# Performance work log

Hardware: AMD Instinct MI355X
Metric: run time of the kernel (lower is better)

## Reference

```python
import jax, jax.numpy as jnp
import numpy as np

B, L = 128, 4096
H, RH, D, K = 128, 64, 64, 512  # num_hiddens, residual_hiddens, embedding_dim, num_embeddings
BETA = 0.25  # commitment_cost


def conv1d(x, w, b=None, stride=1, pad=0):
    # x: (N, C, W); w: (O, I, K) torch layout
    y = jax.lax.conv_general_dilated(x, w, (stride,), [(pad, pad)],
                                     dimension_numbers=('NCW', 'OIW', 'NCW'))
    return y if b is None else y + b[None, :, None]


def convT1d(x, w, b=None, stride=2, pad=1):
    # torch ConvTranspose1d weight layout (in, out, k)
    k = w.shape[-1]
    w_t = jnp.flip(w, -1).transpose(1, 0, 2)  # (out, in, k)
    y = jax.lax.conv_general_dilated(x, w_t, (1,), [(k - 1 - pad, k - 1 - pad)],
                                     lhs_dilation=(stride,),
                                     dimension_numbers=('NCW', 'OIW', 'NCW'))
    return y if b is None else y + b[None, :, None]


def res_stack(x, layers):
    for w1, w2 in layers:
        h = conv1d(jax.nn.relu(x), w1, None, 1, 1)
        h = conv1d(jax.nn.relu(h), w2, None, 1, 0)
        x = x + h
    return jax.nn.relu(x)


def _forward(x, enc_w1, enc_b1, enc_w2, enc_b2, enc_w3, enc_b3,
             enc_r1a, enc_r1b, enc_r2a, enc_r2b, pre_vq_w, pre_vq_b, codebook,
             dec_w1, dec_b1, dec_r1a, dec_r1b, dec_r2a, dec_r2b,
             dec_ct1_w, dec_ct1_b, dec_ct2_w, dec_ct2_b):
    # ---- Encoder (compression_factor == 4) ----
    h = x[:, None, :]                                   # (B, 1, L)
    h = jax.nn.relu(conv1d(h, enc_w1, enc_b1, 2, 1))    # (B, H/2, L/2)
    h = jax.nn.relu(conv1d(h, enc_w2, enc_b2, 2, 1))    # (B, H, L/4)
    h = conv1d(h, enc_w3, enc_b3, 1, 1)
    h = res_stack(h, [(enc_r1a, enc_r1b), (enc_r2a, enc_r2b)])
    z = conv1d(h, pre_vq_w, pre_vq_b, 1, 0)             # (B, D, T)

    # ---- Vector quantization ----
    zt = z.transpose(0, 2, 1)                           # (B, T, D)
    flat = zt.reshape(-1, D)                            # (BT, D)
    dists = (jnp.sum(flat * flat, 1, keepdims=True)
             - 2.0 * flat @ codebook.T
             + jnp.sum(codebook * codebook, 1))         # (BT, K)
    idx = jnp.argmin(dists, axis=1)                     # (BT,)
    q = codebook[idx].reshape(zt.shape)                 # (B, T, D)

    e_latent = jnp.mean((jax.lax.stop_gradient(q) - zt) ** 2)
    q_latent = jnp.mean((q - jax.lax.stop_gradient(zt)) ** 2)
    loss = q_latent + BETA * e_latent
    q_st = zt + jax.lax.stop_gradient(q - zt)           # straight-through

    counts = jnp.zeros((K,), flat.dtype).at[idx].add(1.0)
    probs = counts / idx.shape[0]
    perplexity = jnp.exp(-jnp.sum(probs * jnp.log(probs + 1e-10)))

    # ---- Decoder (compression_factor == 4) ----
    hd = q_st.transpose(0, 2, 1)                        # (B, D, T)
    hd = conv1d(hd, dec_w1, dec_b1, 1, 1)               # (B, H, T)
    hd = res_stack(hd, [(dec_r1a, dec_r1b), (dec_r2a, dec_r2b)])
    hd = jax.nn.relu(convT1d(hd, dec_ct1_w, dec_ct1_b)) # (B, H/2, 2T)
    hd = convT1d(hd, dec_ct2_w, dec_ct2_b)              # (B, 1, 4T)
    recon = jnp.squeeze(hd)                             # (B, L)
    return loss, recon, perplexity


def setup_inputs() -> dict:
    key = jax.random.key(0)
    ks = jax.random.split(key, 32)
    n = lambda i, shape, s=0.05: jax.random.normal(ks[i], shape, jnp.float32) * s
    inp = {
        'x': jax.random.normal(ks[0], (B, L), jnp.float32),
        'enc_w1': n(1, (H // 2, 1, 4)), 'enc_b1': jnp.zeros((H // 2,), jnp.float32),
        'enc_w2': n(2, (H, H // 2, 4)), 'enc_b2': jnp.zeros((H,), jnp.float32),
        'enc_w3': n(3, (H, H, 3)), 'enc_b3': jnp.zeros((H,), jnp.float32),
        'enc_r1a': n(4, (RH, H, 3)), 'enc_r1b': n(5, (H, RH, 1)),
        'enc_r2a': n(6, (RH, H, 3)), 'enc_r2b': n(7, (H, RH, 1)),
        'pre_vq_w': n(8, (D, H, 1)), 'pre_vq_b': jnp.zeros((D,), jnp.float32),
        'codebook': jax.random.uniform(ks[9], (K, D), jnp.float32, -1.0 / K, 1.0 / K),
        'dec_w1': n(10, (H, D, 3)), 'dec_b1': jnp.zeros((H,), jnp.float32),
        'dec_r1a': n(11, (RH, H, 3)), 'dec_r1b': n(12, (H, RH, 1)),
        'dec_r2a': n(13, (RH, H, 3)), 'dec_r2b': n(14, (H, RH, 1)),
        'dec_ct1_w': n(15, (H, H // 2, 4)), 'dec_ct1_b': jnp.zeros((H // 2,), jnp.float32),
        'dec_ct2_w': n(16, (H // 2, 1, 4)), 'dec_ct2_b': jnp.zeros((1,), jnp.float32),
    }
    return inp


def reference(x, enc_w1, enc_b1, enc_w2, enc_b2, enc_w3, enc_b3,
              enc_r1a, enc_r1b, enc_r2a, enc_r2b, pre_vq_w, pre_vq_b, codebook,
              dec_w1, dec_b1, dec_r1a, dec_r1b, dec_r2a, dec_r2b,
              dec_ct1_w, dec_ct1_b, dec_ct2_w, dec_ct2_b):
    return _forward(x, enc_w1, enc_b1, enc_w2, enc_b2, enc_w3, enc_b3,
                    enc_r1a, enc_r1b, enc_r2a, enc_r2b, pre_vq_w, pre_vq_b, codebook,
                    dec_w1, dec_b1, dec_r1a, dec_r1b, dec_r2a, dec_r2b,
                    dec_ct1_w, dec_ct1_b, dec_ct2_w, dec_ct2_b)
```

## Files before the change

### kernel.cpp

```cpp
#include <hip/hip_runtime.h>
#include <hip/hip_bf16.h>
#include <math.h>

using bf16 = __hip_bfloat16;
typedef __attribute__((ext_vector_type(4))) float f32x4;
typedef __attribute__((ext_vector_type(8))) short s16x8;

#define MFMA16(a,b,c) __builtin_amdgcn_mfma_f32_16x16x32_bf16((a),(b),(c),0,0,0)


__device__ inline float bf2f(unsigned short u) {
    union { float f; unsigned v; } c; c.v = ((unsigned)u) << 16; return c.f;
}
__device__ inline unsigned short bfbits(float f) {
    union { bf16 h; unsigned short u; } c; c.h = __float2bfloat16(f); return c.u;
}
__device__ inline s16x8 relu8(s16x8 v) {
#pragma unroll
    for (int j = 0; j < 8; ++j)
        v[j] = (short)(((unsigned short)v[j] & 0x8000u) ? 0 : (unsigned short)v[j]);
    return v;
}

__global__ __launch_bounds__(256) void encmid_k(
    const bf16* __restrict__ in, const bf16* __restrict__ w3t,
    const float* __restrict__ b3, const bf16* __restrict__ r1w1,
    const bf16* __restrict__ r1w2, const bf16* __restrict__ r2w1,
    const bf16* __restrict__ r2w2, bf16* __restrict__ out)
{
    __shared__ bf16 sX[96 * 128];
    __shared__ bf16 sY[80 * 128];
    __shared__ bf16 sH[80 * 64];
    const int tid = threadIdx.x;
    const int b   = blockIdx.y;
    const int l0  = blockIdx.x * 64;
    const bf16* inb = in + (size_t)b * 1024 * 128;

    for (int i = tid; i < 96 * 16; i += 256) {
        int t = i >> 4, c0 = (i & 15) * 8;
        int g = l0 - 16 + t;
        s16x8 v = {};
        if (g >= 0 && g < 1024) v = *(const s16x8*)(inb + (size_t)g * 128 + c0);
        int byte = ((t * 128 + c0) << 1) ^ ((t & 7) << 4);
        *(s16x8*)((char*)sX + byte) = v;
    }
    __syncthreads();

    const int lane = tid & 63;
    const int wid  = __builtin_amdgcn_readfirstlane(tid >> 6);
    const int lr   = lane & 15;
    const int kg   = lane >> 4;
    const f32x4 zf4 = {0.f, 0.f, 0.f, 0.f};

    {
        const int co0 = wid * 32;
        f32x4 acc[2][5];
#pragma unroll
        for (int cf = 0; cf < 2; ++cf)
#pragma unroll
            for (int lf = 0; lf < 5; ++lf) acc[cf][lf] = zf4;
#pragma unroll
        for (int k = 0; k < 3; ++k) {
            const bf16* Ab = w3t + (size_t)k * 128 * 128;
#pragma unroll
            for (int ks = 0; ks < 4; ++ks) {
                s16x8 af[2];
#pragma unroll
                for (int cf = 0; cf < 2; ++cf)
                    af[cf] = *(const s16x8*)(Ab + (co0 + cf * 16 + lr) * 128 + ks * 32 + kg * 8);
                s16x8 bfr[5];
#pragma unroll
                for (int lf = 0; lf < 5; ++lf) {
                    int tx = lf * 16 + lr + 7 + k;
                    int byte = ((tx * 128 + ks * 32 + kg * 8) << 1) ^ ((tx & 7) << 4);
                    bfr[lf] = *(const s16x8*)((const char*)sX + byte);
                }
#pragma unroll
                for (int cf = 0; cf < 2; ++cf)
#pragma unroll
                    for (int lf = 0; lf < 5; ++lf)
                        acc[cf][lf] = MFMA16(af[cf], bfr[lf], acc[cf][lf]);
            }
        }
#pragma unroll
        for (int cf = 0; cf < 2; ++cf)
#pragma unroll
            for (int lf = 0; lf < 5; ++lf) {
                int row = lf * 16 + lr;
                int p   = l0 - 8 + row;
                int cb0 = co0 + cf * 16 + kg * 4;
                bool ok = (p >= 0 && p < 1024);
                float r[4];
#pragma unroll
                for (int j = 0; j < 4; ++j)
                    r[j] = ok ? (acc[cf][lf][j] + b3[cb0 + j]) : 0.f;
                uint2 pk;
                pk.x = (unsigned)bfbits(r[0]) | ((unsigned)bfbits(r[1]) << 16);
                pk.y = (unsigned)bfbits(r[2]) | ((unsigned)bfbits(r[3]) << 16);
                int byte = ((row * 128 + cb0) << 1) ^ ((row & 7) << 4);
                *(uint2*)((char*)sY + byte) = pk;
            }
    }
    __syncthreads();

#pragma unroll 1
    for (int blk = 0; blk < 2; ++blk) {
        const bf16* w1 = blk ? r2w1 : r1w1;
        {
            const int co0 = wid * 16;
            f32x4 acc[5];
#pragma unroll
            for (int lf = 0; lf < 5; ++lf) acc[lf] = zf4;
#pragma unroll
            for (int k = 0; k < 3; ++k) {
                const bf16* Ab = w1 + (size_t)k * 64 * 128;
#pragma unroll
                for (int ks = 0; ks < 4; ++ks) {
                    s16x8 a = *(const s16x8*)(Ab + (co0 + lr) * 128 + ks * 32 + kg * 8);
                    s16x8 bfr[5];
#pragma unroll
                    for (int lf = 0; lf < 5; ++lf) {
                        int ry = lf * 16 + lr + k - 1;
                        ry = (ry < 0) ? 0 : (ry > 79 ? 79 : ry);
                        int byte = ((ry * 128 + ks * 32 + kg * 8) << 1) ^ ((ry & 7) << 4);
                        bfr[lf] = relu8(*(const s16x8*)((const char*)sY + byte));
                    }
#pragma unroll
                    for (int lf = 0; lf < 5; ++lf)
                        acc[lf] = MFMA16(a, bfr[lf], acc[lf]);
                }
            }
#pragma unroll
            for (int lf = 0; lf < 5; ++lf) {
                int row = lf * 16 + lr;
                int ch0 = co0 + kg * 4;
                uint2 pk;
                pk.x = (unsigned)bfbits(fmaxf(acc[lf][0], 0.f)) |
                       ((unsigned)bfbits(fmaxf(acc[lf][1], 0.f)) << 16);
                pk.y = (unsigned)bfbits(fmaxf(acc[lf][2], 0.f)) |
                       ((unsigned)bfbits(fmaxf(acc[lf][3], 0.f)) << 16);
                int byte = ((row * 64 + ch0) << 1) ^ ((row & 7) << 4);
                *(uint2*)((char*)sH + byte) = pk;
            }
        }
        __syncthreads();

        if (blk == 0) {
            const int co0 = wid * 32;
            f32x4 acc[2][5];
#pragma unroll
            for (int cf = 0; cf < 2; ++cf)
#pragma unroll
                for (int lf = 0; lf < 5; ++lf) acc[cf][lf] = zf4;
#pragma unroll
            for (int ks = 0; ks < 2; ++ks) {
                s16x8 af[2];
#pragma unroll
                for (int cf = 0; cf < 2; ++cf)
                    af[cf] = *(const s16x8*)(r1w2 + (size_t)(co0 + cf * 16 + lr) * 64 + ks * 32 + kg * 8);
                s16x8 bfr[5];
#pragma unroll
                for (int lf = 0; lf < 5; ++lf) {
                    int row = lf * 16 + lr;
                    int byte = ((row * 64 + ks * 32 + kg * 8) << 1) ^ ((row & 7) << 4);
                    bfr[lf] = *(const s16x8*)((const char*)sH + byte);
                }
#pragma unroll
                for (int cf = 0; cf < 2; ++cf)
#pragma unroll
                    for (int lf = 0; lf < 5; ++lf)
                        acc[cf][lf] = MFMA16(af[cf], bfr[lf], acc[cf][lf]);
            }
#pragma unroll
            for (int cf = 0; cf < 2; ++cf)
#pragma unroll
                for (int lf = 0; lf < 5; ++lf) {
                    int row = lf * 16 + lr;
                    int p   = l0 - 8 + row;
                    int cb0 = co0 + cf * 16 + kg * 4;
                    int byte = ((row * 128 + cb0) << 1) ^ ((row & 7) << 4);
                    uint2 old = *(const uint2*)((const char*)sY + byte);
                    bool ok = (p >= 0 && p < 1024);
                    float r[4];
                    r[0] = acc[cf][lf][0] + bf2f((unsigned short)(old.x & 0xffff));
                    r[1] = acc[cf][lf][1] + bf2f((unsigned short)(old.x >> 16));
                    r[2] = acc[cf][lf][2] + bf2f((unsigned short)(old.y & 0xffff));
                    r[3] = acc[cf][lf][3] + bf2f((unsigned short)(old.y >> 16));
                    uint2 pk;
                    pk.x = ok ? ((unsigned)bfbits(r[0]) | ((unsigned)bfbits(r[1]) << 16)) : 0u;
                    pk.y = ok ? ((unsigned)bfbits(r[2]) | ((unsigned)bfbits(r[3]) << 16)) : 0u;
                    *(uint2*)((char*)sY + byte) = pk;
                }
            __syncthreads();
        } else {
            const int co0 = wid * 32;
            f32x4 acc[2][4];
#pragma unroll
            for (int cf = 0; cf < 2; ++cf)
#pragma unroll
                for (int lf = 0; lf < 4; ++lf) acc[cf][lf] = zf4;
#pragma unroll
            for (int ks = 0; ks < 2; ++ks) {
                s16x8 af[2];
#pragma unroll
                for (int cf = 0; cf < 2; ++cf)
                    af[cf] = *(const s16x8*)(r2w2 + (size_t)(co0 + cf * 16 + lr) * 64 + ks * 32 + kg * 8);
                s16x8 bfr[4];
#pragma unroll
                for (int lf = 0; lf < 4; ++lf) {
                    int row = 8 + lf * 16 + lr;
                    int byte = ((row * 64 + ks * 32 + kg * 8) << 1) ^ ((row & 7) << 4);
                    bfr[lf] = *(const s16x8*)((const char*)sH + byte);
                }
#pragma unroll
                for (int cf = 0; cf < 2; ++cf)
#pragma unroll
                    for (int lf = 0; lf < 4; ++lf)
                        acc[cf][lf] = MFMA16(af[cf], bfr[lf], acc[cf][lf]);
            }
#pragma unroll
            for (int cf = 0; cf < 2; ++cf)
#pragma unroll
                for (int lf = 0; lf < 4; ++lf) {
                    int row = 8 + lf * 16 + lr;
                    int cb0 = co0 + cf * 16 + kg * 4;
                    int byte = ((row * 128 + cb0) << 1) ^ ((row & 7) << 4);
                    uint2 old = *(const uint2*)((const char*)sY + byte);
                    float r[4];
                    r[0] = fmaxf(acc[cf][lf][0] + bf2f((unsigned short)(old.x & 0xffff)), 0.f);
                    r[1] = fmaxf(acc[cf][lf][1] + bf2f((unsigned short)(old.x >> 16)), 0.f);
                    r[2] = fmaxf(acc[cf][lf][2] + bf2f((unsigned short)(old.y & 0xffff)), 0.f);
                    r[3] = fmaxf(acc[cf][lf][3] + bf2f((unsigned short)(old.y >> 16)), 0.f);
                    uint2 pk;
                    pk.x = (unsigned)bfbits(r[0]) | ((unsigned)bfbits(r[1]) << 16);
                    pk.y = (unsigned)bfbits(r[2]) | ((unsigned)bfbits(r[3]) << 16);
                    *(uint2*)(out + ((size_t)b * 1024 + l0 + lf * 16 + lr) * 128 + cb0) = pk;
                }
        }
    }
}

__global__ __launch_bounds__(256) void decmid_k(
    const bf16* __restrict__ qin, const bf16* __restrict__ dw1,
    const float* __restrict__ db1, const bf16* __restrict__ r1w1,
    const bf16* __restrict__ r1w2, const bf16* __restrict__ r2w1,
    const bf16* __restrict__ r2w2, const bf16* __restrict__ ct1w,
    const float* __restrict__ ct1b, bf16* __restrict__ out)
{
    __shared__ bf16 sQ[96 * 64];
    __shared__ bf16 sY[80 * 128];
    __shared__ bf16 sH[80 * 64];
    const int tid = threadIdx.x;
    const int b   = blockIdx.y;
    const int l0  = blockIdx.x * 64;
    const bf16* inb = qin + (size_t)b * 1024 * 64;

    for (int i = tid; i < 96 * 8; i += 256) {
        int t = i >> 3, c0 = (i & 7) * 8;
        int g = l0 - 16 + t;
        s16x8 v = {};
        if (g >= 0 && g < 1024) v = *(const s16x8*)(inb + (size_t)g * 64 + c0);
        int byte = ((t * 64 + c0) << 1) ^ ((t & 7) << 4);
        *(s16x8*)((char*)sQ + byte) = v;
    }
    __syncthreads();

    const int lane = tid & 63;
    const int wid  = __builtin_amdgcn_readfirstlane(tid >> 6);
    const int lr   = lane & 15;
    const int kg   = lane >> 4;
    const f32x4 zf4 = {0.f, 0.f, 0.f, 0.f};

    {
        const int co0 = wid * 32;
        f32x4 acc[2][5];
#pragma unroll
        for (int cf = 0; cf < 2; ++cf)
#pragma unroll
            for (int lf = 0; lf < 5; ++lf) acc[cf][lf] = zf4;
#pragma unroll
        for (int k = 0; k < 3; ++k) {
            const bf16* Ab = dw1 + (size_t)k * 128 * 64;
#pragma unroll
            for (int ks = 0; ks < 2; ++ks) {
                s16x8 af[2];
#pragma unroll
                for (int cf = 0; cf < 2; ++cf)
                    af[cf] = *(const s16x8*)(Ab + (co0 + cf * 16 + lr) * 64 + ks * 32 + kg * 8);
                s16x8 bfr[5];
#pragma unroll
                for (int lf = 0; lf < 5; ++lf) {
                    int tx = lf * 16 + lr + 7 + k;
                    int byte = ((tx * 64 + ks * 32 + kg * 8) << 1) ^ ((tx & 7) << 4);
                    bfr[lf] = *(const s16x8*)((const char*)sQ + byte);
                }
#pragma unroll
                for (int cf = 0; cf < 2; ++cf)
#pragma unroll
                    for (int lf = 0; lf < 5; ++lf)
                        acc[cf][lf] = MFMA16(af[cf], bfr[lf], acc[cf][lf]);
            }
        }
#pragma unroll
        for (int cf = 0; cf < 2; ++cf)
#pragma unroll
            for (int lf = 0; lf < 5; ++lf) {
                int row = lf * 16 + lr;
                int p   = l0 - 8 + row;
                int cb0 = co0 + cf * 16 + kg * 4;
                bool ok = (p >= 0 && p < 1024);
                float r[4];
#pragma unroll
                for (int j = 0; j < 4; ++j)
                    r[j] = ok ? (acc[cf][lf][j] + db1[cb0 + j]) : 0.f;
                uint2 pk;
                pk.x = (unsigned)bfbits(r[0]) | ((unsigned)bfbits(r[1]) << 16);
                pk.y = (unsigned)bfbits(r[2]) | ((unsigned)bfbits(r[3]) << 16);
                int byte = ((row * 128 + cb0) << 1) ^ ((row & 7) << 4);
                *(uint2*)((char*)sY + byte) = pk;
            }
    }
    __syncthreads();

#pragma unroll 1
    for (int blk = 0; blk < 2; ++blk) {
        const bf16* w1 = blk ? r2w1 : r1w1;
        const bf16* w2 = blk ? r2w2 : r1w2;
        {
            const int co0 = wid * 16;
            f32x4 acc[5];
#pragma unroll
            for (int lf = 0; lf < 5; ++lf) acc[lf] = zf4;
#pragma unroll
            for (int k = 0; k < 3; ++k) {
                const bf16* Ab = w1 + (size_t)k * 64 * 128;
#pragma unroll
                for (int ks = 0; ks < 4; ++ks) {
                    s16x8 a = *(const s16x8*)(Ab + (co0 + lr) * 128 + ks * 32 + kg * 8);
                    s16x8 bfr[5];
#pragma unroll
                    for (int lf = 0; lf < 5; ++lf) {
                        int ry = lf * 16 + lr + k - 1;
                        ry = (ry < 0) ? 0 : (ry > 79 ? 79 : ry);
                        int byte = ((ry * 128 + ks * 32 + kg * 8) << 1) ^ ((ry & 7) << 4);
                        bfr[lf] = relu8(*(const s16x8*)((const char*)sY + byte));
                    }
#pragma unroll
                    for (int lf = 0; lf < 5; ++lf)
                        acc[lf] = MFMA16(a, bfr[lf], acc[lf]);
                }
            }
#pragma unroll
            for (int lf = 0; lf < 5; ++lf) {
                int row = lf * 16 + lr;
                int ch0 = co0 + kg * 4;
                uint2 pk;
                pk.x = (unsigned)bfbits(fmaxf(acc[lf][0], 0.f)) |
                       ((unsigned)bfbits(fmaxf(acc[lf][1], 0.f)) << 16);
                pk.y = (unsigned)bfbits(fmaxf(acc[lf][2], 0.f)) |
                       ((unsigned)bfbits(fmaxf(acc[lf][3], 0.f)) << 16);
                int byte = ((row * 64 + ch0) << 1) ^ ((row & 7) << 4);
                *(uint2*)((char*)sH + byte) = pk;
            }
        }
        __syncthreads();
        {
            const int co0 = wid * 32;
            f32x4 acc[2][5];
#pragma unroll
            for (int cf = 0; cf < 2; ++cf)
#pragma unroll
                for (int lf = 0; lf < 5; ++lf) acc[cf][lf] = zf4;
#pragma unroll
            for (int ks = 0; ks < 2; ++ks) {
                s16x8 af[2];
#pragma unroll
                for (int cf = 0; cf < 2; ++cf)
                    af[cf] = *(const s16x8*)(w2 + (size_t)(co0 + cf * 16 + lr) * 64 + ks * 32 + kg * 8);
                s16x8 bfr[5];
#pragma unroll
                for (int lf = 0; lf < 5; ++lf) {
                    int row = lf * 16 + lr;
                    int byte = ((row * 64 + ks * 32 + kg * 8) << 1) ^ ((row & 7) << 4);
                    bfr[lf] = *(const s16x8*)((const char*)sH + byte);
                }
#pragma unroll
                for (int cf = 0; cf < 2; ++cf)
#pragma unroll
                    for (int lf = 0; lf < 5; ++lf)
                        acc[cf][lf] = MFMA16(af[cf], bfr[lf], acc[cf][lf]);
            }
#pragma unroll
            for (int cf = 0; cf < 2; ++cf)
#pragma unroll
                for (int lf = 0; lf < 5; ++lf) {
                    int row = lf * 16 + lr;
                    int p   = l0 - 8 + row;
                    int cb0 = co0 + cf * 16 + kg * 4;
                    int byte = ((row * 128 + cb0) << 1) ^ ((row & 7) << 4);
                    uint2 old = *(const uint2*)((const char*)sY + byte);
                    bool ok = (p >= 0 && p < 1024);
                    float r[4];
                    r[0] = acc[cf][lf][0] + bf2f((unsigned short)(old.x & 0xffff));
                    r[1] = acc[cf][lf][1] + bf2f((unsigned short)(old.x >> 16));
                    r[2] = acc[cf][lf][2] + bf2f((unsigned short)(old.y & 0xffff));
                    r[3] = acc[cf][lf][3] + bf2f((unsigned short)(old.y >> 16));
                    if (blk == 1)
#pragma unroll
                        for (int j = 0; j < 4; ++j) r[j] = fmaxf(r[j], 0.f);
                    uint2 pk;
                    pk.x = ok ? ((unsigned)bfbits(r[0]) | ((unsigned)bfbits(r[1]) << 16)) : 0u;
                    pk.y = ok ? ((unsigned)bfbits(r[2]) | ((unsigned)bfbits(r[3]) << 16)) : 0u;
                    *(uint2*)((char*)sY + byte) = pk;
                }
        }
        __syncthreads();
    }

    {
        const int co0 = (wid & 1) * 32;
        const int mh  = wid >> 1;
        f32x4 acc[2][2][2];
#pragma unroll
        for (int g = 0; g < 2; ++g)
#pragma unroll
            for (int cf = 0; cf < 2; ++cf)
#pragma unroll
                for (int j = 0; j < 2; ++j) acc[g][cf][j] = zf4;
// ... 1 lines not shown
        for (int g = 0; g < 2; ++g)
#pragma unroll
            for (int k = 0; k < 2; ++k) {
                const bf16* Ab = ct1w + (size_t)(g * 2 + k) * 64 * 128;
                const int doff = (g == 0) ? (k - 1) : k;
#pragma unroll
                for (int ks = 0; ks < 4; ++ks) {
                    s16x8 af[2];
#pragma unroll
                    for (int cf = 0; cf < 2; ++cf)
                        af[cf] = *(const s16x8*)(Ab + (co0 + cf * 16 + lr) * 128 + ks * 32 + kg * 8);
                    s16x8 bfr[2];
#pragma unroll
                    for (int j = 0; j < 2; ++j) {
                        int ty = 8 + (mh * 2 + j) * 16 + lr + doff;
                        int byte = ((ty * 128 + ks * 32 + kg * 8) << 1) ^ ((ty & 7) << 4);
                        bfr[j] = *(const s16x8*)((const char*)sY + byte);
                    }
#pragma unroll
                    for (int cf = 0; cf < 2; ++cf)
#pragma unroll
                        for (int j = 0; j < 2; ++j)
                            acc[g][cf][j] = MFMA16(af[cf], bfr[j], acc[g][cf][j]);
                }
            }
#pragma unroll
        for (int g = 0; g < 2; ++g)
#pragma unroll
            for (int cf = 0; cf < 2; ++cf)
#pragma unroll
                for (int j = 0; j < 2; ++j) {
                    int m   = (mh * 2 + j) * 16 + lr;
// ... 6 lines not shown
                    pk.x = (unsigned)bfbits(r[0]) | ((unsigned)bfbits(r[1]) << 16);
                    pk.y = (unsigned)bfbits(r[2]) | ((unsigned)bfbits(r[3]) << 16);
                    *(uint2*)(out + ((size_t)b * 2048 + 2 * (l0 + m) + g) * 64 + cb0) = pk;
                }
    }
}

__global__ __launch_bounds__(256) void enc12_k(
    const float* __restrict__ x, const float* __restrict__ w1,
    const float* __restrict__ b1, const bf16* __restrict__ w2t,
    const float* __restrict__ b2, bf16* __restrict__ out)
{
    __shared__ float sXf[268];
    __shared__ float sW1[256];
    __shared__ float sB1[64];
    __shared__ bf16 sX[132 * 64];
    const int tid = threadIdx.x;
    const int b   = blockIdx.y;
    const int l0  = blockIdx.x * 64;
    const float* xb = x + (size_t)b * 4096;

    for (int i = tid; i < 266; i += 256) {
        int g = 4 * l0 - 3 + i;
        sXf[i] = (g >= 0 && g < 4096) ? xb[g] : 0.f;
    }
    if (tid < 256) sW1[tid] = w1[tid];
    if (tid < 64)  sB1[tid] = b1[tid];
    __syncthreads();

    for (int i = tid; i < 132 * 64; i += 256) {
        int t = i >> 6, c = i & 63;
        int p = (t < 66) ? 2 * (l0 + t) : 2 * (l0 + t - 66) - 1;
        float v = 0.f;
        if (p >= 0 && p < 2048) {
            int xi = 2 * p - 4 * l0 + 2;
            float a = sB1[c];
#pragma unroll
            for (int k = 0; k < 4; ++k) a = fmaf(sXf[xi + k], sW1[c * 4 + k], a);
            v = fmaxf(a, 0.f);
        }
        int byte = ((t * 64 + c) << 1) ^ ((t & 7) << 4);
        *(bf16*)((char*)sX + byte) = __float2bfloat16(v);
    }
    __syncthreads();

    const int lane = tid & 63;
    const int wid  = __builtin_amdgcn_readfirstlane(tid >> 6);
    const int co0  = wid * 32;
    const int lr   = lane & 15;
    const int kg   = lane >> 4;

    f32x4 acc[2][4];
#pragma unroll
    for (int cf = 0; cf < 2; ++cf)
#pragma unroll
        for (int lf = 0; lf < 4; ++lf) acc[cf][lf] = (f32x4){0.f, 0.f, 0.f, 0.f};

#pragma unroll
    for (int k = 0; k < 4; ++k) {
        const int roff = (k == 0) ? 66 : (k == 1) ? 0 : (k == 2) ? 67 : 1;
        const bf16* Ab = w2t + (size_t)k * 128 * 64;
#pragma unroll
        for (int ks = 0; ks < 2; ++ks) {
            s16x8 af[2];
#pragma unroll
            for (int cf = 0; cf < 2; ++cf)
                af[cf] = *(const s16x8*)(Ab + (co0 + cf * 16 + lr) * 64 + ks * 32 + kg * 8);
            s16x8 bfr[4];
#pragma unroll
            for (int lf = 0; lf < 4; ++lf) {
                int t = roff + lf * 16 + lr;
                int byte = ((t * 64 + ks * 32 + kg * 8) << 1) ^ ((t & 7) << 4);
                bfr[lf] = *(const s16x8*)((const char*)sX + byte);
            }
#pragma unroll
            for (int cf = 0; cf < 2; ++cf)
#pragma unroll
                for (int lf = 0; lf < 4; ++lf)
                    acc[cf][lf] = MFMA16(af[cf], bfr[lf], acc[cf][lf]);
        }
    }

#pragma unroll
    for (int cf = 0; cf < 2; ++cf)
#pragma unroll
        for (int lf = 0; lf < 4; ++lf) {
            int cb0  = co0 + cf * 16 + kg * 4;
            int lcol = lf * 16 + lr;
            float r[4];
#pragma unroll
            for (int j = 0; j < 4; ++j)
                r[j] = fmaxf(acc[cf][lf][j] + b2[cb0 + j], 0.f);
            uint2 pk;
            pk.x = (unsigned)bfbits(r[0]) | ((unsigned)bfbits(r[1]) << 16);
            pk.y = (unsigned)bfbits(r[2]) | ((unsigned)bfbits(r[3]) << 16);
            *(uint2*)(out + ((size_t)b * 1024 + l0 + lcol) * 128 + cb0) = pk;
        }
}

__global__ __launch_bounds__(256) void ct2_k(
    const bf16* __restrict__ in, const float* __restrict__ w,
    const float* __restrict__ bias, float* __restrict__ out)
{
    __shared__ bf16 sX[258 * 64];
    const int tid = threadIdx.x;
    const int b   = blockIdx.y;
    const int m0  = blockIdx.x * 256;
    const bf16* inb = in + (size_t)b * 2048 * 64;
    for (int i = tid; i < 258 * 8; i += 256) {
        int t = i >> 3, c0 = (i & 7) * 8;
        int g = m0 - 1 + t;
        s16x8 v = {};
        if (g >= 0 && g < 2048) v = *(const s16x8*)(inb + (size_t)g * 64 + c0);
        int byte = ((t * 64 + c0) << 1) ^ ((t & 7) << 4);
        *(s16x8*)((char*)sX + byte) = v;
    }
    __syncthreads();
    float e = bias[0], o = bias[0];
#pragma unroll
    for (int c0 = 0; c0 < 64; c0 += 8) {
        int t0 = tid, t1 = tid + 1, t2 = tid + 2;
        s16x8 vm1 = *(const s16x8*)((char*)sX + (((t0 * 64 + c0) << 1) ^ ((t0 & 7) << 4)));
        s16x8 v0  = *(const s16x8*)((char*)sX + (((t1 * 64 + c0) << 1) ^ ((t1 & 7) << 4)));
        s16x8 vp1 = *(const s16x8*)((char*)sX + (((t2 * 64 + c0) << 1) ^ ((t2 & 7) << 4)));
#pragma unroll
        for (int j = 0; j < 8; ++j) {
            int ci = c0 + j;
            float xm1 = bf2f((unsigned short)vm1[j]);
            float x0  = bf2f((unsigned short)v0[j]);
            float xp1 = bf2f((unsigned short)vp1[j]);
            e = fmaf(x0,  w[ci * 4 + 1], fmaf(xm1, w[ci * 4 + 3], e));
            o = fmaf(xp1, w[ci * 4 + 0], fmaf(x0,  w[ci * 4 + 2], o));
        }
    }
    int m = m0 + tid;
    out[(size_t)b * 4096 + 2 * m]     = e;
    out[(size_t)b * 4096 + 2 * m + 1] = o;
}

// ... 49 lines not shown
#pragma unroll
    for (int c0 = 0; c0 < 64; c0 += 8) {
        union { unsigned short u[8]; s16x8 v; } ph, pl;
#pragma unroll
        for (int j = 0; j < 8; ++j) {
            float v = c[c0 + j];
            unsigned short h = bfbits(v);
            ph.u[j] = h;
            pl.u[j] = bfbits(v - bf2f(h));
        }
        *(s16x8*)(cbh + (size_t)k * 64 + c0) = ph.v;
        *(s16x8*)(cbl + (size_t)k * 64 + c0) = pl.v;
    }
}

__global__ __launch_bounds__(256) void vqf_k(
    const bf16* __restrict__ A, const bf16* __restrict__ pvw,
    const float* __restrict__ pvb, const float* __restrict__ cbf,
    const bf16* __restrict__ cbh, const bf16* __restrict__ cbl,
    const float* __restrict__ sc, bf16* __restrict__ q,
    float* __restrict__ counts, float* __restrict__ loss_sum)
{
    __shared__ s16x8 sMemV[4096];
    char* sMem = (char*)sMemV;
    __shared__ float sSC[512];
    __shared__ float sHist[512];
    __shared__ int   sBK[256];
    __shared__ float sWS[4];
    const int tid = threadIdx.x;
    sSC[tid] = sc[tid]; sSC[tid + 256] = sc[tid + 256];
    sHist[tid] = 0.f;   sHist[tid + 256] = 0.f;

    const int n0blk = blockIdx.x * 256;
    for (int i = tid; i < 256 * 16; i += 256) {
        int t = i >> 4, c0 = (i & 15) * 8;
        s16x8 v = *(const s16x8*)(A + (size_t)(n0blk + t) * 128 + c0);
        int byte = ((t * 128 + c0) << 1) ^ ((t & 7) << 4);
        *(s16x8*)(sMem + byte) = v;
    }
    __syncthreads();

    const int lane = tid & 63, wid = tid >> 6;
    const int lr = lane & 15, kg = lane >> 4;
    const int pw0 = wid * 64;
    const f32x4 zf4 = {0.f, 0.f, 0.f, 0.f};

    f32x4 zacc[4][4];
#pragma unroll
    for (int cf = 0; cf < 4; ++cf)
#pragma unroll
        for (int lf = 0; lf < 4; ++lf) zacc[cf][lf] = zf4;
#pragma unroll
    for (int ks = 0; ks < 4; ++ks) {
        s16x8 af[4];
#pragma unroll
        for (int cf = 0; cf < 4; ++cf)
            af[cf] = *(const s16x8*)(pvw + (size_t)(cf * 16 + lr) * 128 + ks * 32 + kg * 8);
        s16x8 bfr[4];
#pragma unroll
        for (int lf = 0; lf < 4; ++lf) {
            int t = pw0 + lf * 16 + lr;
            int byte = ((t * 128 + ks * 32 + kg * 8) << 1) ^ ((t & 7) << 4);
            bfr[lf] = *(const s16x8*)((const char*)sMem + byte);
        }
#pragma unroll
        for (int cf = 0; cf < 4; ++cf)
#pragma unroll
            for (int lf = 0; lf < 4; ++lf)
                zacc[cf][lf] = MFMA16(af[cf], bfr[lf], zacc[cf][lf]);
    }
    __syncthreads();

#pragma unroll
    for (int cf = 0; cf < 4; ++cf)
#pragma unroll
        for (int lf = 0; lf < 4; ++lf) {
            int pos = pw0 + lf * 16 + lr;
            int ch  = cf * 16 + kg * 4;
            float4 v = make_float4(zacc[cf][lf][0] + pvb[ch],
                                   zacc[cf][lf][1] + pvb[ch + 1],
                                   zacc[cf][lf][2] + pvb[ch + 2],
                                   zacc[cf][lf][3] + pvb[ch + 3]);
            int byte = ((pos * 64 + ch) << 2) ^ ((pos & 7) << 5);
            *(float4*)(sMem + byte) = v;
        }
    __syncthreads();

    s16x8 bh[4][2], bl[4][2];
#pragma unroll
    for (int lf = 0; lf < 4; ++lf)
#pragma unroll
        for (int ks = 0; ks < 2; ++ks) {
            int t = pw0 + lf * 16 + lr;
            int ch = ks * 32 + kg * 8;
            int byte = ((t * 64 + ch) << 2) ^ ((t & 7) << 5);
            float4 v0 = *(const float4*)(sMem + byte);
            float4 v1 = *(const float4*)(sMem + byte + 16);
            float v[8] = {v0.x, v0.y, v0.z, v0.w, v1.x, v1.y, v1.z, v1.w};
            union { unsigned short u[8]; s16x8 s; } ph, pl;
#pragma unroll
            for (int j = 0; j < 8; ++j) {
                unsigned short h = bfbits(v[j]);
                ph.u[j] = h;
                pl.u[j] = bfbits(v[j] - bf2f(h));
            }
            bh[lf][ks] = ph.s; bl[lf][ks] = pl.s;
        }

    float bestd[4] = {3.4e38f, 3.4e38f, 3.4e38f, 3.4e38f};
    int   bestk[4] = {0, 0, 0, 0};
#pragma unroll 2
    for (int cf = 0; cf < 32; ++cf) {
        int code = cf * 16 + lr;
        const bf16* ph = cbh + code * 64 + kg * 8;
        const bf16* pl = cbl + code * 64 + kg * 8;
        s16x8 ah0 = *(const s16x8*)ph;
        s16x8 ah1 = *(const s16x8*)(ph + 32);
        s16x8 al0 = *(const s16x8*)pl;
        s16x8 al1 = *(const s16x8*)(pl + 32);
        float s0 = sSC[cf * 16 + kg * 4 + 0];
        float s1 = sSC[cf * 16 + kg * 4 + 1];
        float s2 = sSC[cf * 16 + kg * 4 + 2];
        float s3 = sSC[cf * 16 + kg * 4 + 3];
        int kb = cf * 16 + kg * 4;
#pragma unroll
        for (int lf = 0; lf < 4; ++lf) {
            f32x4 acc = MFMA16(ah0, bh[lf][0], zf4);
            acc = MFMA16(ah1, bh[lf][1], acc);
            acc = MFMA16(al0, bh[lf][0], acc);
            acc = MFMA16(al1, bh[lf][1], acc);
            acc = MFMA16(ah0, bl[lf][0], acc);
            acc = MFMA16(ah1, bl[lf][1], acc);
            float d0 = fmaf(acc[0], -2.f, s0);
            float d1 = fmaf(acc[1], -2.f, s1);
            float d2 = fmaf(acc[2], -2.f, s2);
            float d3 = fmaf(acc[3], -2.f, s3);
            if (d0 < bestd[lf]) { bestd[lf] = d0; bestk[lf] = kb; }
            if (d1 < bestd[lf]) { bestd[lf] = d1; bestk[lf] = kb + 1; }
            if (d2 < bestd[lf]) { bestd[lf] = d2; bestk[lf] = kb + 2; }
            if (d3 < bestd[lf]) { bestd[lf] = d3; bestk[lf] = kb + 3; }
        }
    }
#pragma unroll
    for (int lf = 0; lf < 4; ++lf) {
#pragma unroll
        for (int off = 16; off <= 32; off <<= 1) {
            float od = __shfl_xor(bestd[lf], off, 64);
            int   ok = __shfl_xor(bestk[lf], off, 64);
            if (od < bestd[lf] || (od == bestd[lf] && ok < bestk[lf])) {
                bestd[lf] = od; bestk[lf] = ok;
            }
        }
        if (kg == 0) sBK[wid * 64 + lf * 16 + lr] = bestk[lf];
    }
    __syncthreads();

    const int n = n0blk + tid;
    const int k = sBK[tid];
    atomicAdd(&sHist[k], 1.f);
    float lsum = 0.f;
    const float* qp = cbf + (size_t)k * 64;
#pragma unroll
    for (int c0 = 0; c0 < 64; c0 += 8) {
        int byte = ((tid * 64 + c0) << 2) ^ ((tid & 7) << 5);
        float4 z0 = *(const float4*)(sMem + byte);
        float4 z1 = *(const float4*)(sMem + byte + 16);
        float4 q0 = *(const float4*)(qp + c0);
        float4 q1 = *(const float4*)(qp + c0 + 4);
        float qv[8] = {q0.x, q0.y, q0.z, q0.w, q1.x, q1.y, q1.z, q1.w};
        float zv[8] = {z0.x, z0.y, z0.z, z0.w, z1.x, z1.y, z1.z, z1.w};
        union { unsigned short u[8]; s16x8 v; } pk;
#pragma unroll
        for (int j = 0; j < 8; ++j) {
            float d = qv[j] - zv[j];
            lsum = fmaf(d, d, lsum);
            pk.u[j] = bfbits(qv[j]);
        }
        *(s16x8*)(q + (size_t)n * 64 + c0) = pk.v;
    }
#pragma unroll
    for (int off = 32; off > 0; off >>= 1) lsum += __shfl_down(lsum, off, 64);
    if ((tid & 63) == 0) sWS[tid >> 6] = lsum;
    __syncthreads();
    if (tid == 0) atomicAdd(loss_sum, sWS[0] + sWS[1] + sWS[2] + sWS[3]);
    float c0v = sHist[tid];       if (c0v != 0.f) atomicAdd(&counts[tid], c0v);
    float c1v = sHist[tid + 256]; if (c1v != 0.f) atomicAdd(&counts[tid + 256], c1v);
}

__global__ __launch_bounds__(512) void finalize_k(
    const float* __restrict__ counts, const float* __restrict__ loss_sum,
    float* __restrict__ d_out, int out_size)
{
    __shared__ float ws2[8];
// ... 29 lines not shown
    const float* ct2_w    = (const float*)d_in[22];
    const float* ct2_b    = (const float*)d_in[23];
    float* out = (float*)d_out;

    char* base = (char*)d_ws;
    bf16*  wb   = (bf16*)base;
    bf16*  Abf  = (bf16*)(base + ((size_t)2   << 20));
    bf16*  Bbf  = (bf16*)(base + ((size_t)40  << 20));
    bf16*  Qbf  = (bf16*)(base + ((size_t)78  << 20));
    bf16*  cbh  = (bf16*)(base + ((size_t)96  << 20));
    bf16*  cbl  = (bf16*)(base + ((size_t)96  << 20) + 65536);
    float* sc   = (float*)(base + ((size_t)96  << 20) + 131072);
    float* cnt  = sc + 512;
    float* lsum = cnt + 512;

    hipMemsetAsync(cnt, 0, 513 * sizeof(float), stream);

    dim3 blk(256);
    dim3 g16(16, 128);

    wx_k<<<dim3(13, 8), blk, 0, stream>>>(
        (const float*)d_in[3], (const float*)d_in[5], (const float*)d_in[7],
        (const float*)d_in[8], (const float*)d_in[9], (const float*)d_in[10],
        (const float*)d_in[11], (const float*)d_in[14], (const float*)d_in[16],
        (const float*)d_in[17], (const float*)d_in[18], (const float*)d_in[19],
        (const float*)d_in[20], wb);
    cbprep_k<<<2, blk, 0, stream>>>(cb, cbh, cbl, sc);

    enc12_k<<<g16, blk, 0, stream>>>(x, enc_w1, enc_b1, wb + 0 * 65536, enc_b2, Bbf);
    encmid_k<<<g16, blk, 0, stream>>>(Bbf, wb + 1 * 65536, enc_b3,
        wb + 2 * 65536, wb + 3 * 65536, wb + 4 * 65536, wb + 5 * 65536, Abf);

    vqf_k<<<512, blk, 0, stream>>>(Abf, wb + 6 * 65536, pre_vq_b, cb,
                                   cbh, cbl, sc, Qbf, cnt, lsum);

    decmid_k<<<g16, blk, 0, stream>>>(Qbf, wb + 7 * 65536, dec_b1,
        wb + 8 * 65536, wb + 9 * 65536, wb + 10 * 65536, wb + 11 * 65536,
        wb + 12 * 65536, ct1_b, Bbf);

    ct2_k<<<dim3(8, 128), blk, 0, stream>>>(Bbf, ct2_w, ct2_b, out + 1);
    finalize_k<<<1, 512, 0, stream>>>(cnt, lsum, out, out_size);
}
```

Measured before the change: 358.6 us.

## Shrink LDS footprint via buffer aliasing and padded rows, halve VQ tile

Replaces the XOR-swizzled shared-memory layouts with padded row strides (136/72 elements) and aliases the input staging buffer with the hidden buffer in encmid_k and decmid_k, adding a barrier before the overwrite. Adds launch-bounds occupancy hints. The VQ kernel now handles 128 positions per block, launched on twice as many blocks, and uses two threads per position in the epilogue. The aim is to cut LDS use so more blocks fit per CU and latency is better hidden. The cost is an extra barrier, register pressure from the min-blocks hints, and possible bank conflicts from padding instead of swizzling.

```diff
diff --git a/kernel.cpp b/kernel.cpp
--- a/kernel.cpp
+++ b/kernel.cpp
@@ -22,15 +22,16 @@
     return v;
 }
 
-__global__ __launch_bounds__(256) void encmid_k(
+__global__ __launch_bounds__(256, 3) void encmid_k(
     const bf16* __restrict__ in, const bf16* __restrict__ w3t,
     const float* __restrict__ b3, const bf16* __restrict__ r1w1,
     const bf16* __restrict__ r1w2, const bf16* __restrict__ r2w1,
     const bf16* __restrict__ r2w2, bf16* __restrict__ out)
 {
-    __shared__ bf16 sX[96 * 128];
-    __shared__ bf16 sY[80 * 128];
-    __shared__ bf16 sH[80 * 64];
+    __shared__ __align__(16) char smem[47872];
+    char* sY = smem;
+    char* sX = smem + 21760;
+    char* sH = smem + 21760;
     const int tid = threadIdx.x;
     const int b   = blockIdx.y;
     const int l0  = blockIdx.x * 64;
@@ -41,8 +42,7 @@
         int g = l0 - 16 + t;
         s16x8 v = {};
         if (g >= 0 && g < 1024) v = *(const s16x8*)(inb + (size_t)g * 128 + c0);
-        int byte = ((t * 128 + c0) << 1) ^ ((t & 7) << 4);
-        *(s16x8*)((char*)sX + byte) = v;
+        *(s16x8*)(sX + ((t * 136 + c0) << 1)) = v;
     }
     __syncthreads();
 
@@ -72,8 +72,7 @@
 #pragma unroll
                 for (int lf = 0; lf < 5; ++lf) {
                     int tx = lf * 16 + lr + 7 + k;
-                    int byte = ((tx * 128 + ks * 32 + kg * 8) << 1) ^ ((tx & 7) << 4);
-                    bfr[lf] = *(const s16x8*)((const char*)sX + byte);
+                    bfr[lf] = *(const s16x8*)(sX + ((tx * 136 + ks * 32 + kg * 8) << 1));
                 }
 #pragma unroll
                 for (int cf = 0; cf < 2; ++cf)
@@ -82,6 +81,7 @@
                         acc[cf][lf] = MFMA16(af[cf], bfr[lf], acc[cf][lf]);
             }
         }
+        __syncthreads();
 #pragma unroll
         for (int cf = 0; cf < 2; ++cf)
 #pragma unroll
@@ -97,8 +97,7 @@
                 uint2 pk;
                 pk.x = (unsigned)bfbits(r[0]) | ((unsigned)bfbits(r[1]) << 16);
                 pk.y = (unsigned)bfbits(r[2]) | ((unsigned)bfbits(r[3]) << 16);
-                int byte = ((row * 128 + cb0) << 1) ^ ((row & 7) << 4);
-                *(uint2*)((char*)sY + byte) = pk;
+                *(uint2*)(sY + ((row * 136 + cb0) << 1)) = pk;
             }
     }
     __syncthreads();
@@ -122,8 +121,7 @@
                     for (int lf = 0; lf < 5; ++lf) {
                         int ry = lf * 16 + lr + k - 1;
                         ry = (ry < 0) ? 0 : (ry > 79 ? 79 : ry);
-                        int byte = ((ry * 128 + ks * 32 + kg * 8) << 1) ^ ((ry & 7) << 4);
-                        bfr[lf] = relu8(*(const s16x8*)((const char*)sY + byte));
+                        bfr[lf] = relu8(*(const s16x8*)(sY + ((ry * 136 + ks * 32 + kg * 8) << 1)));
                     }
 #pragma unroll
                     for (int lf = 0; lf < 5; ++lf)
@@ -139,8 +137,7 @@
                        ((unsigned)bfbits(fmaxf(acc[lf][1], 0.f)) << 16);
                 pk.y = (unsigned)bfbits(fmaxf(acc[lf][2], 0.f)) |
                        ((unsigned)bfbits(fmaxf(acc[lf][3], 0.f)) << 16);
-                int byte = ((row * 64 + ch0) << 1) ^ ((row & 7) << 4);
-                *(uint2*)((char*)sH + byte) = pk;
+                *(uint2*)(sH + ((row * 72 + ch0) << 1)) = pk;
             }
         }
         __syncthreads();
@@ -162,8 +159,7 @@
 #pragma unroll
                 for (int lf = 0; lf < 5; ++lf) {
                     int row = lf * 16 + lr;
-                    int byte = ((row * 64 + ks * 32 + kg * 8) << 1) ^ ((row & 7) << 4);
-                    bfr[lf] = *(const s16x8*)((const char*)sH + byte);
+                    bfr[lf] = *(const s16x8*)(sH + ((row * 72 + ks * 32 + kg * 8) << 1));
                 }
 #pragma unroll
                 for (int cf = 0; cf < 2; ++cf)
@@ -178,8 +174,7 @@
                     int row = lf * 16 + lr;
                     int p   = l0 - 8 + row;
                     int cb0 = co0 + cf * 16 + kg * 4;
-                    int byte = ((row * 128 + cb0) << 1) ^ ((row & 7) << 4);
-                    uint2 old = *(const uint2*)((const char*)sY + byte);
+                    uint2 old = *(const uint2*)(sY + ((row * 136 + cb0) << 1));
                     bool ok = (p >= 0 && p < 1024);
                     float r[4];
                     r[0] = acc[cf][lf][0] + bf2f((unsigned short)(old.x & 0xffff));
@@ -189,7 +184,7 @@
                     uint2 pk;
                     pk.x = ok ? ((unsigned)bfbits(r[0]) | ((unsigned)bfbits(r[1]) << 16)) : 0u;
                     pk.y = ok ? ((unsigned)bfbits(r[2]) | ((unsigned)bfbits(r[3]) << 16)) : 0u;
-                    *(uint2*)((char*)sY + byte) = pk;
+                    *(uint2*)(sY + ((row * 136 + cb0) << 1)) = pk;
                 }
             __syncthreads();
         } else {
@@ -209,8 +204,7 @@
 #pragma unroll
                 for (int lf = 0; lf < 4; ++lf) {
                     int row = 8 + lf * 16 + lr;
-                    int byte = ((row * 64 + ks * 32 + kg * 8) << 1) ^ ((row & 7) << 4);
-                    bfr[lf] = *(const s16x8*)((const char*)sH + byte);
+                    bfr[lf] = *(const s16x8*)(sH + ((row * 72 + ks * 32 + kg * 8) << 1));
                 }
 #pragma unroll
                 for (int cf = 0; cf < 2; ++cf)
@@ -224,8 +218,7 @@
                 for (int lf = 0; lf < 4; ++lf) {
                     int row = 8 + lf * 16 + lr;
                     int cb0 = co0 + cf * 16 + kg * 4;
-                    int byte = ((row * 128 + cb0) << 1) ^ ((row & 7) << 4);
-                    uint2 old = *(const uint2*)((const char*)sY + byte);
+                    uint2 old = *(const uint2*)(sY + ((row * 136 + cb0) << 1));
                     float r[4];
                     r[0] = fmaxf(acc[cf][lf][0] + bf2f((unsigned short)(old.x & 0xffff)), 0.f);
                     r[1] = fmaxf(acc[cf][lf][1] + bf2f((unsigned short)(old.x >> 16)), 0.f);
@@ -240,16 +233,17 @@
     }
 }
 
-__global__ __launch_bounds__(256) void decmid_k(
+__global__ __launch_bounds__(256, 4) void decmid_k(
     const bf16* __restrict__ qin, const bf16* __restrict__ dw1,
     const float* __restrict__ db1, const bf16* __restrict__ r1w1,
     const bf16* __restrict__ r1w2, const bf16* __restrict__ r2w1,
     const bf16* __restrict__ r2w2, const bf16* __restrict__ ct1w,
     const float* __restrict__ ct1b, bf16* __restrict__ out)
 {
-    __shared__ bf16 sQ[96 * 64];
-    __shared__ bf16 sY[80 * 128];
-    __shared__ bf16 sH[80 * 64];
+    __shared__ __align__(16) char smem[35584];
+    char* sY = smem;
+    char* sQ = smem + 21760;
+    char* sH = smem + 21760;
     const int tid = threadIdx.x;
     const int b   = blockIdx.y;
     const int l0  = blockIdx.x * 64;
@@ -260,8 +254,7 @@
         int g = l0 - 16 + t;
         s16x8 v = {};
         if (g >= 0 && g < 1024) v = *(const s16x8*)(inb + (size_t)g * 64 + c0);
-        int byte = ((t * 64 + c0) << 1) ^ ((t & 7) << 4);
-        *(s16x8*)((char*)sQ + byte) = v;
+        *(s16x8*)(sQ + ((t * 72 + c0) << 1)) = v;
     }
     __syncthreads();
 
@@ -291,8 +284,7 @@
 #pragma unroll
                 for (int lf = 0; lf < 5; ++lf) {
                     int tx = lf * 16 + lr + 7 + k;
-                    int byte = ((tx * 64 + ks * 32 + kg * 8) << 1) ^ ((tx & 7) << 4);
-                    bfr[lf] = *(const s16x8*)((const char*)sQ + byte);
+                    bfr[lf] = *(const s16x8*)(sQ + ((tx * 72 + ks * 32 + kg * 8) << 1));
                 }
 #pragma unroll
                 for (int cf = 0; cf < 2; ++cf)
@@ -301,6 +293,7 @@
                         acc[cf][lf] = MFMA16(af[cf], bfr[lf], acc[cf][lf]);
             }
         }
+        __syncthreads();
 #pragma unroll
         for (int cf = 0; cf < 2; ++cf)
 #pragma unroll
@@ -316,8 +309,7 @@
                 uint2 pk;
                 pk.x = (unsigned)bfbits(r[0]) | ((unsigned)bfbits(r[1]) << 16);
                 pk.y = (unsigned)bfbits(r[2]) | ((unsigned)bfbits(r[3]) << 16);
-                int byte = ((row * 128 + cb0) << 1) ^ ((row & 7) << 4);
-                *(uint2*)((char*)sY + byte) = pk;
+                *(uint2*)(sY + ((row * 136 + cb0) << 1)) = pk;
             }
     }
     __syncthreads();
@@ -342,8 +334,7 @@
                     for (int lf = 0; lf < 5; ++lf) {
                         int ry = lf * 16 + lr + k - 1;
                         ry = (ry < 0) ? 0 : (ry > 79 ? 79 : ry);
-                        int byte = ((ry * 128 + ks * 32 + kg * 8) << 1) ^ ((ry & 7) << 4);
-                        bfr[lf] = relu8(*(const s16x8*)((const char*)sY + byte));
+                        bfr[lf] = relu8(*(const s16x8*)(sY + ((ry * 136 + ks * 32 + kg * 8) << 1)));
                     }
 #pragma unroll
                     for (int lf = 0; lf < 5; ++lf)
@@ -359,8 +350,7 @@
                        ((unsigned)bfbits(fmaxf(acc[lf][1], 0.f)) << 16);
                 pk.y = (unsigned)bfbits(fmaxf(acc[lf][2], 0.f)) |
                        ((unsigned)bfbits(fmaxf(acc[lf][3], 0.f)) << 16);
-                int byte = ((row * 64 + ch0) << 1) ^ ((row & 7) << 4);
-                *(uint2*)((char*)sH + byte) = pk;
+                *(uint2*)(sH + ((row * 72 + ch0) << 1)) = pk;
             }
         }
         __syncthreads();
@@ -381,8 +371,7 @@
 #pragma unroll
                 for (int lf = 0; lf < 5; ++lf) {
                     int row = lf * 16 + lr;
-                    int byte = ((row * 64 + ks * 32 + kg * 8) << 1) ^ ((row & 7) << 4);
-                    bfr[lf] = *(const s16x8*)((const char*)sH + byte);
+                    bfr[lf] = *(const s16x8*)(sH + ((row * 72 + ks * 32 + kg * 8) << 1));
                 }
 #pragma unroll
                 for (int cf = 0; cf < 2; ++cf)
@@ -397,8 +386,7 @@
                     int row = lf * 16 + lr;
                     int p   = l0 - 8 + row;
                     int cb0 = co0 + cf * 16 + kg * 4;
-                    int byte = ((row * 128 + cb0) << 1) ^ ((row & 7) << 4);
-                    uint2 old = *(const uint2*)((const char*)sY + byte);
+                    uint2 old = *(const uint2*)(sY + ((row * 136 + cb0) << 1));
                     bool ok = (p >= 0 && p < 1024);
                     float r[4];
                     r[0] = acc[cf][lf][0] + bf2f((unsigned short)(old.x & 0xffff));
@@ -411,7 +399,7 @@
                     uint2 pk;
                     pk.x = ok ? ((unsigned)bfbits(r[0]) | ((unsigned)bfbits(r[1]) << 16)) : 0u;
                     pk.y = ok ? ((unsigned)bfbits(r[2]) | ((unsigned)bfbits(r[3]) << 16)) : 0u;
-                    *(uint2*)((char*)sY + byte) = pk;
+                    *(uint2*)(sY + ((row * 136 + cb0) << 1)) = pk;
                 }
         }
         __syncthreads();
@@ -443,8 +431,7 @@
 #pragma unroll
                     for (int j = 0; j < 2; ++j) {
                         int ty = 8 + (mh * 2 + j) * 16 + lr + doff;
-                        int byte = ((ty * 128 + ks * 32 + kg * 8) << 1) ^ ((ty & 7) << 4);
-                        bfr[j] = *(const s16x8*)((const char*)sY + byte);
+                        bfr[j] = *(const s16x8*)(sY + ((ty * 136 + ks * 32 + kg * 8) << 1));
                     }
 #pragma unroll
                     for (int cf = 0; cf < 2; ++cf)
@@ -481,7 +468,7 @@
     __shared__ float sXf[268];
     __shared__ float sW1[256];
     __shared__ float sB1[64];
-    __shared__ bf16 sX[132 * 64];
+    __shared__ __align__(16) char sX[132 * 144];
     const int tid = threadIdx.x;
     const int b   = blockIdx.y;
     const int l0  = blockIdx.x * 64;
@@ -506,8 +493,7 @@
             for (int k = 0; k < 4; ++k) a = fmaf(sXf[xi + k], sW1[c * 4 + k], a);
             v = fmaxf(a, 0.f);
         }
-        int byte = ((t * 64 + c) << 1) ^ ((t & 7) << 4);
-        *(bf16*)((char*)sX + byte) = __float2bfloat16(v);
+        *(bf16*)(sX + ((t * 72 + c) << 1)) = __float2bfloat16(v);
     }
     __syncthreads();
 
@@ -537,8 +523,7 @@
 #pragma unroll
             for (int lf = 0; lf < 4; ++lf) {
                 int t = roff + lf * 16 + lr;
-                int byte = ((t * 64 + ks * 32 + kg * 8) << 1) ^ ((t & 7) << 4);
-                bfr[lf] = *(const s16x8*)((const char*)sX + byte);
+                bfr[lf] = *(const s16x8*)(sX + ((t * 72 + ks * 32 + kg * 8) << 1));
             }
 #pragma unroll
             for (int cf = 0; cf < 2; ++cf)
@@ -569,7 +554,7 @@
     const bf16* __restrict__ in, const float* __restrict__ w,
     const float* __restrict__ bias, float* __restrict__ out)
 {
-    __shared__ bf16 sX[258 * 64];
+    __shared__ __align__(16) char sX[258 * 144];
     const int tid = threadIdx.x;
     const int b   = blockIdx.y;
     const int m0  = blockIdx.x * 256;
@@ -579,17 +564,15 @@
         int g = m0 - 1 + t;
         s16x8 v = {};
         if (g >= 0 && g < 2048) v = *(const s16x8*)(inb + (size_t)g * 64 + c0);
-        int byte = ((t * 64 + c0) << 1) ^ ((t & 7) << 4);
-        *(s16x8*)((char*)sX + byte) = v;
+        *(s16x8*)(sX + ((t * 72 + c0) << 1)) = v;
     }
     __syncthreads();
     float e = bias[0], o = bias[0];
 #pragma unroll
     for (int c0 = 0; c0 < 64; c0 += 8) {
-        int t0 = tid, t1 = tid + 1, t2 = tid + 2;
-        s16x8 vm1 = *(const s16x8*)((char*)sX + (((t0 * 64 + c0) << 1) ^ ((t0 & 7) << 4)));
-        s16x8 v0  = *(const s16x8*)((char*)sX + (((t1 * 64 + c0) << 1) ^ ((t1 & 7) << 4)));
-        s16x8 vp1 = *(const s16x8*)((char*)sX + (((t2 * 64 + c0) << 1) ^ ((t2 & 7) << 4)));
+        s16x8 vm1 = *(const s16x8*)(sX + (((tid + 0) * 72 + c0) << 1));
+        s16x8 v0  = *(const s16x8*)(sX + (((tid + 1) * 72 + c0) << 1));
+        s16x8 vp1 = *(const s16x8*)(sX + (((tid + 2) * 72 + c0) << 1));
 #pragma unroll
         for (int j = 0; j < 8; ++j) {
             int ci = c0 + j;
@@ -669,59 +652,56 @@
     }
 }
 
-__global__ __launch_bounds__(256) void vqf_k(
+__global__ __launch_bounds__(256, 4) void vqf_k(
     const bf16* __restrict__ A, const bf16* __restrict__ pvw,
     const float* __restrict__ pvb, const float* __restrict__ cbf,
     const bf16* __restrict__ cbh, const bf16* __restrict__ cbl,
     const float* __restrict__ sc, bf16* __restrict__ q,
     float* __restrict__ counts, float* __restrict__ loss_sum)
 {
-    __shared__ s16x8 sMemV[4096];
-    char* sMem = (char*)sMemV;
+    __shared__ __align__(16) char sMem[34816];
     __shared__ float sSC[512];
     __shared__ float sHist[512];
-    __shared__ int   sBK[256];
+    __shared__ int   sBK[128];
     __shared__ float sWS[4];
     const int tid = threadIdx.x;
     sSC[tid] = sc[tid]; sSC[tid + 256] = sc[tid + 256];
     sHist[tid] = 0.f;   sHist[tid + 256] = 0.f;
 
-    const int n0blk = blockIdx.x * 256;
-    for (int i = tid; i < 256 * 16; i += 256) {
+    const int n0 = blockIdx.x * 128;
+    for (int i = tid; i < 128 * 16; i += 256) {
         int t = i >> 4, c0 = (i & 15) * 8;
-        s16x8 v = *(const s16x8*)(A + (size_t)(n0blk + t) * 128 + c0);
-        int byte = ((t * 128 + c0) << 1) ^ ((t & 7) << 4);
-        *(s16x8*)(sMem + byte) = v;
+        s16x8 v = *(const s16x8*)(A + (size_t)(n0 + t) * 128 + c0);
+        *(s16x8*)(sMem + ((t * 136 + c0) << 1)) = v;
     }
     __syncthreads();
 
     const int lane = tid & 63, wid = tid >> 6;
     const int lr = lane & 15, kg = lane >> 4;
-    const int pw0 = wid * 64;
+    const int pw0 = wid * 32;
     const f32x4 zf4 = {0.f, 0.f, 0.f, 0.f};
 
-    f32x4 zacc[4][4];
+    f32x4 zacc[4][2];
 #pragma unroll
     for (int cf = 0; cf < 4; ++cf)
 #pragma unroll
-        for (int lf = 0; lf < 4; ++lf) zacc[cf][lf] = zf4;
+        for (int lf = 0; lf < 2; ++lf) zacc[cf][lf] = zf4;
 #pragma unroll
     for (int ks = 0; ks < 4; ++ks) {
         s16x8 af[4];
 #pragma unroll
         for (int cf = 0; cf < 4; ++cf)
             af[cf] = *(const s16x8*)(pvw + (size_t)(cf * 16 + lr) * 128 + ks * 32 + kg * 8);
-        s16x8 bfr[4];
-#pragma unroll
-        for (int lf = 0; lf < 4; ++lf) {
+        s16x8 bfr[2];
+#pragma unroll
+        for (int lf = 0; lf < 2; ++lf) {
             int t = pw0 + lf * 16 + lr;
-            int byte = ((t * 128 + ks * 32 + kg * 8) << 1) ^ ((t & 7) << 4);
-            bfr[lf] = *(const s16x8*)((const char*)sMem + byte);
+            bfr[lf] = *(const s16x8*)(sMem + ((t * 136 + ks * 32 + kg * 8) << 1));
         }
 #pragma unroll
         for (int cf = 0; cf < 4; ++cf)
 #pragma unroll
-            for (int lf = 0; lf < 4; ++lf)
+            for (int lf = 0; lf < 2; ++lf)
                 zacc[cf][lf] = MFMA16(af[cf], bfr[lf], zacc[cf][lf]);
     }
     __syncthreads();
@@ -729,28 +709,26 @@
 #pragma unroll
     for (int cf = 0; cf < 4; ++cf)
 #pragma unroll
-        for (int lf = 0; lf < 4; ++lf) {
+        for (int lf = 0; lf < 2; ++lf) {
             int pos = pw0 + lf * 16 + lr;
             int ch  = cf * 16 + kg * 4;
             float4 v = make_float4(zacc[cf][lf][0] + pvb[ch],
                                    zacc[cf][lf][1] + pvb[ch + 1],
                                    zacc[cf][lf][2] + pvb[ch + 2],
                                    zacc[cf][lf][3] + pvb[ch + 3]);
-            int byte = ((pos * 64 + ch) << 2) ^ ((pos & 7) << 5);
-            *(float4*)(sMem + byte) = v;
-        }
-    __syncthreads();
-
-    s16x8 bh[4][2], bl[4][2];
-#pragma unroll
-    for (int lf = 0; lf < 4; ++lf)
+            *(float4*)(sMem + (pos * 68 + ch) * 4) = v;
+        }
+    __syncthreads();
+
+    s16x8 bh[2][2], bl[2][2];
+#pragma unroll
+    for (int lf = 0; lf < 2; ++lf)
 #pragma unroll
         for (int ks = 0; ks < 2; ++ks) {
             int t = pw0 + lf * 16 + lr;
             int ch = ks * 32 + kg * 8;
-            int byte = ((t * 64 + ch) << 2) ^ ((t & 7) << 5);
-            float4 v0 = *(const float4*)(sMem + byte);
-            float4 v1 = *(const float4*)(sMem + byte + 16);
+            float4 v0 = *(const float4*)(sMem + (t * 68 + ch) * 4);
+            float4 v1 = *(const float4*)(sMem + (t * 68 + ch) * 4 + 16);
             float v[8] = {v0.x, v0.y, v0.z, v0.w, v1.x, v1.y, v1.z, v1.w};
             union { unsigned short u[8]; s16x8 s; } ph, pl;
 #pragma unroll
@@ -762,8 +740,8 @@
             bh[lf][ks] = ph.s; bl[lf][ks] = pl.s;
         }
 
-    float bestd[4] = {3.4e38f, 3.4e38f, 3.4e38f, 3.4e38f};
-    int   bestk[4] = {0, 0, 0, 0};
+    float bestd[2] = {3.4e38f, 3.4e38f};
+    int   bestk[2] = {0, 0};
 #pragma unroll 2
     for (int cf = 0; cf < 32; ++cf) {
         int code = cf * 16 + lr;
@@ -779,7 +757,7 @@
         float s3 = sSC[cf * 16 + kg * 4 + 3];
         int kb = cf * 16 + kg * 4;
 #pragma unroll
-        for (int lf = 0; lf < 4; ++lf) {
+        for (int lf = 0; lf < 2; ++lf) {
             f32x4 acc = MFMA16(ah0, bh[lf][0], zf4);
             acc = MFMA16(ah1, bh[lf][1], acc);
             acc = MFMA16(al0, bh[lf][0], acc);
@@ -797,7 +775,7 @@
         }
     }
 #pragma unroll
-    for (int lf = 0; lf < 4; ++lf) {
+    for (int lf = 0; lf < 2; ++lf) {
 #pragma unroll
         for (int off = 16; off <= 32; off <<= 1) {
             float od = __shfl_xor(bestd[lf], off, 64);
@@ -806,20 +784,22 @@
                 bestd[lf] = od; bestk[lf] = ok;
             }
         }
-        if (kg == 0) sBK[wid * 64 + lf * 16 + lr] = bestk[lf];
-    }
-    __syncthreads();
-
-    const int n = n0blk + tid;
-    const int k = sBK[tid];
-    atomicAdd(&sHist[k], 1.f);
+        if (kg == 0) sBK[pw0 + lf * 16 + lr] = bestk[lf];
+    }
+    __syncthreads();
+
+    const int pos  = tid >> 1;
+    const int half = tid & 1;
+    const int k = sBK[pos];
+    if (half == 0) atomicAdd(&sHist[k], 1.f);
     float lsum = 0.f;
-    const float* qp = cbf + (size_t)k * 64;
-#pragma unroll
-    for (int c0 = 0; c0 < 64; c0 += 8) {
-        int byte = ((tid * 64 + c0) << 2) ^ ((tid & 7) << 5);
-        float4 z0 = *(const float4*)(sMem + byte);
-        float4 z1 = *(const float4*)(sMem + byte + 16);
+    const float* qp = cbf + (size_t)k * 64 + half * 32;
+    bf16* qo = q + (size_t)(n0 + pos) * 64 + half * 32;
+#pragma unroll
+    for (int c0 = 0; c0 < 32; c0 += 8) {
+        int zb = (pos * 68 + half * 32 + c0) * 4;
+        float4 z0 = *(const float4*)(sMem + zb);
+        float4 z1 = *(const float4*)(sMem + zb + 16);
         float4 q0 = *(const float4*)(qp + c0);
         float4 q1 = *(const float4*)(qp + c0 + 4);
         float qv[8] = {q0.x, q0.y, q0.z, q0.w, q1.x, q1.y, q1.z, q1.w};
@@ -831,7 +811,7 @@
             lsum = fmaf(d, d, lsum);
             pk.u[j] = bfbits(qv[j]);
         }
-        *(s16x8*)(q + (size_t)n * 64 + c0) = pk.v;
+        *(s16x8*)(qo + c0) = pk.v;
     }
 #pragma unroll
     for (int off = 32; off > 0; off >>= 1) lsum += __shfl_down(lsum, off, 64);
@@ -891,7 +871,7 @@
     float* cnt  = sc + 512;
     float* lsum = cnt + 512;
 
-    hipMemsetAsync(cnt, 0, 513 * sizeof(float), stream);
+    (void)hipMemsetAsync(cnt, 0, 513 * sizeof(float), stream);
 
     dim3 blk(256);
     dim3 g16(16, 128);
@@ -908,8 +888,8 @@
     encmid_k<<<g16, blk, 0, stream>>>(Bbf, wb + 1 * 65536, enc_b3,
         wb + 2 * 65536, wb + 3 * 65536, wb + 4 * 65536, wb + 5 * 65536, Abf);
 
-    vqf_k<<<512, blk, 0, stream>>>(Abf, wb + 6 * 65536, pre_vq_b, cb,
-                                   cbh, cbl, sc, Qbf, cnt, lsum);
+    vqf_k<<<1024, blk, 0, stream>>>(Abf, wb + 6 * 65536, pre_vq_b, cb,
+                                    cbh, cbl, sc, Qbf, cnt, lsum);
 
     decmid_k<<<g16, blk, 0, stream>>>(Qbf, wb + 7 * 65536, dec_b1,
         wb + 8 * 65536, wb + 9 * 65536, wb + 10 * 65536, wb + 11 * 65536,
```

After: 357.6 us. About the same (-0.3%).
